# Optimization experiments

Hardware: AMD Instinct MI355X
Metric: run time of the kernel (lower is better)

The kernel has to match this reference:

```python
import jax, jax.numpy as jnp
import numpy as np

H, C, L = 4, 64, 3          # heads, out_channels, conv layers
N, E, B = 20000, 320000, 32 # nodes, edges, graphs
HD = 64                     # hidden_dim


def setup_inputs() -> dict:
    key = jax.random.key(0)
    ks = jax.random.split(key, 24)
    x = jax.random.normal(ks[0], (N, 3), jnp.float32)
    src = jax.random.randint(ks[1], (E,), 0, N)
    dst = jax.random.randint(ks[2], (E,), 0, N)
    dst = jnp.where(dst == src, (dst + 1) % N, dst)  # no pre-existing self loops
    edge_index = jnp.stack([src, dst])
    edge_attr = jax.random.normal(ks[3], (E, 4), jnp.float32)
    u = jax.random.normal(ks[4], (B, 10), jnp.float32)
    batch = jnp.sort(jax.random.randint(ks[5], (N,), 0, B))
    p = lambda k, s: jax.random.normal(k, s, jnp.float32) * 0.1
    return {
        'x': x, 'edge_index': edge_index, 'edge_attr': edge_attr, 'u': u, 'batch': batch,
        'node_W': p(ks[6], (3, HD)), 'node_b': p(ks[7], (HD,)),
        'eemb_W': p(ks[8], (4, HD)), 'eemb_b': p(ks[9], (HD,)),
        'lin_W': p(ks[10], (L, HD, H * C)),
        'att_src': p(ks[11], (L, H, C)), 'att_dst': p(ks[12], (L, H, C)),
        'lin_eW': p(ks[13], (L, HD, H * C)), 'att_e': p(ks[14], (L, H, C)),
        'conv_b': p(ks[15], (L, C)),
        'gW': p(ks[16], (10, HD)), 'gb': p(ks[17], (HD,)),
        'f1W': p(ks[18], (2 * HD, HD)), 'f1b': p(ks[19], (HD,)),
        'f2W': p(ks[20], (HD, 2)), 'f2b': p(ks[21], (2,)),
    }


def _gat_layer(x, src, dst, ea, W, a_src, a_dst, We, a_e, b):
    # PyG GATConv(hidden, hidden, edge_dim=hidden, heads=4, concat=False), eval mode
    n = x.shape[0]
    # add self loops; self-loop edge_attr = mean of incoming edge_attr (fill_value='mean')
    deg = jax.ops.segment_sum(jnp.ones_like(dst, dtype=x.dtype), dst, num_segments=n)
    ea_self = jax.ops.segment_sum(ea, dst, num_segments=n) / jnp.maximum(deg, 1.0)[:, None]
    loop = jnp.arange(n)
    src2 = jnp.concatenate([src, loop])
    dst2 = jnp.concatenate([dst, loop])
    ea2 = jnp.concatenate([ea, ea_self], axis=0)
    xp = (x @ W).reshape(n, H, C)                       # [N,H,C]
    a_s = jnp.einsum('nhc,hc->nh', xp, a_src)           # [N,H]
    a_d = jnp.einsum('nhc,hc->nh', xp, a_dst)
    ee = (ea2 @ We).reshape(-1, H, C)                   # [E2,H,C]
    a_ed = jnp.einsum('ehc,hc->eh', ee, a_e)
    alpha = jax.nn.leaky_relu(a_s[src2] + a_d[dst2] + a_ed, 0.2)  # [E2,H]
    # segment softmax over destination nodes (stable)
    m = jax.ops.segment_max(alpha, dst2, num_segments=n)
    ex = jnp.exp(alpha - m[dst2])
    den = jax.ops.segment_sum(ex, dst2, num_segments=n)
    att = ex / den[dst2]
    out = jax.ops.segment_sum(xp[src2] * att[..., None], dst2, num_segments=n)  # [N,H,C]
    return out.mean(axis=1) + b  # concat=False -> mean over heads


def reference(x, edge_index, edge_attr, u, batch, node_W, node_b, eemb_W, eemb_b,
              lin_W, att_src, att_dst, lin_eW, att_e, conv_b, gW, gb, f1W, f1b, f2W, f2b):
    src, dst = edge_index[0], edge_index[1]
    h = jax.nn.relu(x @ node_W + node_b)
    ea = jax.nn.relu(edge_attr @ eemb_W + eemb_b)
    for i in range(L):
        h = jax.nn.relu(_gat_layer(h, src, dst, ea, lin_W[i], att_src[i], att_dst[i],
                                   lin_eW[i], att_e[i], conv_b[i]))
    # global mean pool over graphs
    cnt = jax.ops.segment_sum(jnp.ones((h.shape[0],), h.dtype), batch, num_segments=B)
    pooled = jax.ops.segment_sum(h, batch, num_segments=B) / jnp.maximum(cnt, 1.0)[:, None]
    ug = jax.nn.relu(u @ gW + gb)
    z = jnp.concatenate([pooled, ug], axis=1)
    z = jax.nn.relu(z @ f1W + f1b)
    return z @ f2W + f2b
```

## Files before the change

kernel.cpp:

```cpp
#include <hip/hip_runtime.h>
#include <hip/hip_bf16.h>

#define HD 64

typedef unsigned short u16;

__device__ __forceinline__ float lrelu(float x) { return x > 0.f ? x : 0.2f * x; }
__device__ __forceinline__ int clampi(int v, int maxv) {
    return v < 0 ? 0 : (v >= maxv ? maxv - 1 : v);
}
__device__ __forceinline__ float bf2f(u16 u) {
    return __uint_as_float(((unsigned int)u) << 16);
}
__device__ __forceinline__ u16 f2bf(float f) {
    unsigned int u = __float_as_uint(f);
    unsigned int lsb = (u >> 16) & 1u;
    u += 0x7fffu + lsb;
    return (u16)(u >> 16);
}

__global__ void k_init(int* deg, int* cursor, int* gcnt, float* pooled, int N, int B) {
    int i = blockIdx.x * blockDim.x + threadIdx.x;
    if (i < N) { deg[i] = 0; cursor[i] = 0; }
    if (i < B) gcnt[i] = 0;
    if (i < B * HD) pooled[i] = 0.f;
}

__global__ void k_node_emb(const float* __restrict__ x, const float* __restrict__ W,
                           const float* __restrict__ b, float* __restrict__ h, int N) {
    int i = blockIdx.x * blockDim.x + threadIdx.x;
    if (i >= N * HD) return;
    int n = i >> 6, c = i & 63;
    float acc = b[c];
    acc = fmaf(x[n * 3 + 0], W[0 * HD + c], acc);
    acc = fmaf(x[n * 3 + 1], W[1 * HD + c], acc);
    acc = fmaf(x[n * 3 + 2], W[2 * HD + c], acc);
    h[i] = fmaxf(acc, 0.f);
}

__global__ void k_deg(const int* __restrict__ dst, int* __restrict__ deg, int E, int N) {
    int e = blockIdx.x * blockDim.x + threadIdx.x;
    if (e < E) atomicAdd(&deg[clampi(dst[e], N)], 1);
}

__global__ void k_scan1(const int* __restrict__ deg, int* __restrict__ tmp,
                        int* __restrict__ bsum, int N) {
    __shared__ int s[256];
    int tid = threadIdx.x;
    int i = blockIdx.x * 256 + tid;
    int v = (i < N) ? deg[i] : 0;
    s[tid] = v;
    __syncthreads();
    for (int off = 1; off < 256; off <<= 1) {
        int t = (tid >= off) ? s[tid - off] : 0;
        __syncthreads();
        s[tid] += t;
        __syncthreads();
    }
    if (i < N) tmp[i] = s[tid];
    if (tid == 255) bsum[blockIdx.x] = s[255];
}
__global__ void k_scan2(const int* __restrict__ bsum, int* __restrict__ boff, int nb) {
    __shared__ int s[1024];
    int tid = threadIdx.x;
    int v = (tid < nb) ? bsum[tid] : 0;
    s[tid] = v;
    __syncthreads();
    for (int off = 1; off < 1024; off <<= 1) {
        int t = (tid >= off) ? s[tid - off] : 0;
        __syncthreads();
        s[tid] += t;
        __syncthreads();
    }
    if (tid < nb) boff[tid] = s[tid] - v;
}
__global__ void k_scan3(const int* __restrict__ tmp, const int* __restrict__ boff,
                        int* __restrict__ row_ptr, int N) {
    int i = blockIdx.x * blockDim.x + threadIdx.x;
    if (i == 0) row_ptr[0] = 0;
    if (i < N) row_ptr[i + 1] = tmp[i] + boff[i >> 8];
}

__global__ void k_csr(const int* __restrict__ src, const int* __restrict__ dst,
                      const int* __restrict__ row_ptr, int* __restrict__ cursor,
                      int* __restrict__ csr_src, int* __restrict__ csr_dst,
                      int* __restrict__ csr_eid, int E, int N) {
    int e = blockIdx.x * blockDim.x + threadIdx.x;
    if (e >= E) return;
    int d = clampi(dst[e], N);
    int pos = row_ptr[d] + atomicAdd(&cursor[d], 1);
    if (pos < E) {
        csr_src[pos] = clampi(src[e], N);
        csr_dst[pos] = d;
        csr_eid[pos] = e;
    }
}

#define MAXB 2048
__global__ void k_gse(const int* __restrict__ batch, int* __restrict__ gcnt, int N, int B) {
    __shared__ int s_cnt[MAXB];
    int t = threadIdx.x;
    int Bc = B < MAXB ? B : MAXB;
    for (int i = t; i < Bc; i += blockDim.x) s_cnt[i] = 0;
    __syncthreads();
    int n = blockIdx.x * blockDim.x + t;
    if (n < N) {
        int b = clampi(batch[n], B);
        if (b < MAXB) atomicAdd(&s_cnt[b], 1);
        else atomicAdd(&gcnt[b], 1);
    }
    __syncthreads();
    for (int i = t; i < Bc; i += blockDim.x)
        if (s_cnt[i] != 0) atomicAdd(&gcnt[i], s_cnt[i]);
}

__global__ __launch_bounds__(256) void k_ee(
    const float* __restrict__ edge_attr, const float* __restrict__ eW,
    const float* __restrict__ eB, const float* __restrict__ lin_eW,
    const float* __restrict__ att_e, const int* __restrict__ csr_eid,
    float* __restrict__ aed, int E) {
    __shared__ float s_ew[256];
    __shared__ float s_eb[64];
    __shared__ float s_wred[768];
    int t = threadIdx.x;
    s_ew[t] = eW[t];
    if (t < 64) s_eb[t] = eB[t];
    for (int idx = t; idx < 768; idx += 256) {
        int l = idx >> 8, hd = idx & 255, hh = hd >> 6, d = hd & 63;
        const float* We = lin_eW + (size_t)l * HD * 256;
        const float* ae = att_e + (size_t)l * 256;
        float acc = 0.f;
        for (int c = 0; c < 64; c++)
            acc = fmaf(We[d * 256 + hh * 64 + c], ae[hh * 64 + c], acc);
        s_wred[idx] = acc;
    }
    __syncthreads();
    int j0 = (blockIdx.x * 256 + t) * 4;
    if (j0 >= E) return;
    float4 a[4];
    int nv = 0;
    #pragma unroll
    for (int q = 0; q < 4; q++) {
        int j = j0 + q;
        if (j < E) {
            a[q] = *(const float4*)(edge_attr + (size_t)csr_eid[j] * 4);
            nv = q + 1;
        } else {
            a[q] = make_float4(0.f, 0.f, 0.f, 0.f);
        }
    }
    float acc[4][12];
    #pragma unroll
    for (int q = 0; q < 4; q++)
        #pragma unroll
        for (int m = 0; m < 12; m++) acc[q][m] = 0.f;
    for (int k = 0; k < HD; k++) {
        float e0 = s_ew[k], e1 = s_ew[64 + k], e2 = s_ew[128 + k], e3 = s_ew[192 + k];
        float eb = s_eb[k];
        float w[12];
        #pragma unroll
        for (int m = 0; m < 12; m++)
            w[m] = s_wred[(m >> 2) * 256 + (m & 3) * 64 + k];
        #pragma unroll
        for (int q = 0; q < 4; q++) {
            float v = fmaf(a[q].x, e0, fmaf(a[q].y, e1,
                      fmaf(a[q].z, e2, fmaf(a[q].w, e3, eb))));
            v = fmaxf(v, 0.f);
            #pragma unroll
            for (int m = 0; m < 12; m++) acc[q][m] = fmaf(v, w[m], acc[q][m]);
        }
    }
    #pragma unroll
    for (int q = 0; q < 4; q++) {
        if (q >= nv) break;
        float* o = aed + (size_t)(j0 + q) * 12;
        #pragma unroll
        for (int m = 0; m < 12; m++) o[m] = acc[q][m];
    }
}

__global__ void k_selfed(const int* __restrict__ row_ptr, float* __restrict__ aed,
                         int E, int N) {
    int n = blockIdx.x * blockDim.x + threadIdx.x;
    if (n >= N) return;
    int r0 = row_ptr[n], r1 = row_ptr[n + 1];
    float acc[12];
    #pragma unroll
    for (int m = 0; m < 12; m++) acc[m] = 0.f;
    for (int j = r0; j < r1; j++) {
        const float* p = aed + (size_t)j * 12;
        #pragma unroll
        for (int m = 0; m < 12; m++) acc[m] += p[m];
    }
    float inv = 1.f / fmaxf((float)(r1 - r0), 1.f);
    float* o = aed + (size_t)(E + n) * 12;
    #pragma unroll
    for (int m = 0; m < 12; m++) o[m] = acc[m] * inv;
}

__global__ __launch_bounds__(256) void k_xp(
    const float* __restrict__ h, const float* __restrict__ W,
    const float* __restrict__ asrc, const float* __restrict__ adst,
    u16* __restrict__ xp, float* __restrict__ a_s, float* __restrict__ a_d, int N) {
    __shared__ float hs[8 * HD];
    int n0 = blockIdx.x * 8;
    int t = threadIdx.x;
    for (int i = t; i < 8 * HD; i += 256) {
        int nn = n0 + (i >> 6);
        hs[i] = (nn < N) ? h[(size_t)nn * HD + (i & 63)] : 0.f;
    }
    __syncthreads();
    int c = t;
    float acc[8];
    #pragma unroll
    for (int k = 0; k < 8; k++) acc[k] = 0.f;
    for (int d = 0; d < HD; d++) {
        float wv = W[d * 256 + c];
        #pragma unroll
        for (int k = 0; k < 8; k++) acc[k] = fmaf(hs[k * HD + d], wv, acc[k]);
    }
    float as_ = asrc[c], ad_ = adst[c];
    int hh = c >> 6, cc = c & 63;
    #pragma unroll
    for (int k = 0; k < 8; k++) {
        int nn = n0 + k;
        float ps = acc[k] * as_;
        float pd = acc[k] * ad_;
        #pragma unroll
        for (int o = 32; o > 0; o >>= 1) {
            ps += __shfl_xor(ps, o);
            pd += __shfl_xor(pd, o);
        }
        if (nn < N) {
            xp[(size_t)nn * 256 + c] = f2bf(acc[k]);
            if (cc == 0) { a_s[nn * 4 + hh] = ps; a_d[nn * 4 + hh] = pd; }
        }
    }
}

__global__ void k_w(const int* __restrict__ csr_src, const int* __restrict__ csr_dst,
                    const float* __restrict__ aed, const float* __restrict__ a_s,
                    const float* __restrict__ a_d, float* __restrict__ wcsr,
                    int layer, int E, int N) {
    int j = blockIdx.x * blockDim.x + threadIdx.x;
    if (j >= E + N) return;
    int s, d;
    if (j < E) { s = csr_src[j]; d = csr_dst[j]; }
    else       { s = j - E; d = s; }
    const float* p = aed + (size_t)j * 12 + layer * 4;
    float4 as4 = *(const float4*)(a_s + s * 4);
    float4 ad4 = *(const float4*)(a_d + d * 4);
    float w0 = __expf(lrelu(as4.x + ad4.x + p[0]));
    float w1 = __expf(lrelu(as4.y + ad4.y + p[1]));
    float w2 = __expf(lrelu(as4.z + ad4.z + p[2]));
    float w3 = __expf(lrelu(as4.w + ad4.w + p[3]));
    *(float4*)(wcsr + (size_t)j * 4) = make_float4(w0, w1, w2, w3);
}

__global__ __launch_bounds__(256) void k_gat(
    const u16* __restrict__ xp, const float* __restrict__ wcsr,
    const int* __restrict__ row_ptr, const int* __restrict__ csr_src,
    const float* __restrict__ convb, float* __restrict__ h_out, int N, int E) {
    int wave = threadIdx.x >> 6, lane = threadIdx.x & 63;
    int n = blockIdx.x * 4 + wave;
    if (n >= N) return;
    int g = lane >> 4, p = lane & 15;
    int r0 = row_ptr[n], r1 = row_ptr[n + 1];
    float a00 = 0.f, a01 = 0.f, a02 = 0.f, a03 = 0.f;
    float a10 = 0.f, a11 = 0.f, a12 = 0.f, a13 = 0.f;
    float a20 = 0.f, a21 = 0.f, a22 = 0.f, a23 = 0.f;
    float a30 = 0.f, a31 = 0.f, a32 = 0.f, a33 = 0.f;
    float d0 = 0.f, d1 = 0.f, d2 = 0.f, d3 = 0.f;
    if (g == 0) {
        float4 w = *(const float4*)(wcsr + (size_t)(E + n) * 4);
        const u16* row = xp + (size_t)n * 256 + p * 4;
        ushort4 v0 = *(const ushort4*)(row);
        ushort4 v1 = *(const ushort4*)(row + 64);
        ushort4 v2 = *(const ushort4*)(row + 128);
        ushort4 v3 = *(const ushort4*)(row + 192);
        d0 += w.x; d1 += w.y; d2 += w.z; d3 += w.w;
        a00 = fmaf(w.x, bf2f(v0.x), a00); a01 = fmaf(w.x, bf2f(v0.y), a01);
        a02 = fmaf(w.x, bf2f(v0.z), a02); a03 = fmaf(w.x, bf2f(v0.w), a03);
        a10 = fmaf(w.y, bf2f(v1.x), a10); a11 = fmaf(w.y, bf2f(v1.y), a11);
        a12 = fmaf(w.y, bf2f(v1.z), a12); a13 = fmaf(w.y, bf2f(v1.w), a13);
        a20 = fmaf(w.z, bf2f(v2.x), a20); a21 = fmaf(w.z, bf2f(v2.y), a21);
        a22 = fmaf(w.z, bf2f(v2.z), a22); a23 = fmaf(w.z, bf2f(v2.w), a23);
        a30 = fmaf(w.w, bf2f(v3.x), a30); a31 = fmaf(w.w, bf2f(v3.y), a31);
        a32 = fmaf(w.w, bf2f(v3.z), a32); a33 = fmaf(w.w, bf2f(v3.w), a33);
    }
    for (int j = r0 + g; j < r1; j += 4) {
        float4 w = *(const float4*)(wcsr + (size_t)j * 4);
        const u16* row = xp + (size_t)csr_src[j] * 256 + p * 4;
        ushort4 v0 = *(const ushort4*)(row);
        ushort4 v1 = *(const ushort4*)(row + 64);
        ushort4 v2 = *(const ushort4*)(row + 128);
        ushort4 v3 = *(const ushort4*)(row + 192);
        d0 += w.x; d1 += w.y; d2 += w.z; d3 += w.w;
        a00 = fmaf(w.x, bf2f(v0.x), a00); a01 = fmaf(w.x, bf2f(v0.y), a01);
        a02 = fmaf(w.x, bf2f(v0.z), a02); a03 = fmaf(w.x, bf2f(v0.w), a03);
        a10 = fmaf(w.y, bf2f(v1.x), a10); a11 = fmaf(w.y, bf2f(v1.y), a11);
        a12 = fmaf(w.y, bf2f(v1.z), a12); a13 = fmaf(w.y, bf2f(v1.w), a13);
        a20 = fmaf(w.z, bf2f(v2.x), a20); a21 = fmaf(w.z, bf2f(v2.y), a21);
        a22 = fmaf(w.z, bf2f(v2.z), a22); a23 = fmaf(w.z, bf2f(v2.w), a23);
        a30 = fmaf(w.w, bf2f(v3.x), a30); a31 = fmaf(w.w, bf2f(v3.y), a31);
        a32 = fmaf(w.w, bf2f(v3.z), a32); a33 = fmaf(w.w, bf2f(v3.w), a33);
    }
    d0 += __shfl_xor(d0, 16); d0 += __shfl_xor(d0, 32);
    d1 += __shfl_xor(d1, 16); d1 += __shfl_xor(d1, 32);
    d2 += __shfl_xor(d2, 16); d2 += __shfl_xor(d2, 32);
    d3 += __shfl_xor(d3, 16); d3 += __shfl_xor(d3, 32);
    float i0 = 1.f / d0, i1 = 1.f / d1, i2 = 1.f / d2, i3 = 1.f / d3;
    float m0 = a00 * i0 + a10 * i1 + a20 * i2 + a30 * i3;
    float m1 = a01 * i0 + a11 * i1 + a21 * i2 + a31 * i3;
    float m2 = a02 * i0 + a12 * i1 + a22 * i2 + a32 * i3;
    float m3 = a03 * i0 + a13 * i1 + a23 * i2 + a33 * i3;
    m0 += __shfl_xor(m0, 16); m0 += __shfl_xor(m0, 32);
    m1 += __shfl_xor(m1, 16); m1 += __shfl_xor(m1, 32);
    m2 += __shfl_xor(m2, 16); m2 += __shfl_xor(m2, 32);
    m3 += __shfl_xor(m3, 16); m3 += __shfl_xor(m3, 32);
    if (lane < 16) {
        int c = p * 4;
        h_out[(size_t)n * HD + c + 0] = fmaxf(0.25f * m0 + convb[c + 0], 0.f);
        h_out[(size_t)n * HD + c + 1] = fmaxf(0.25f * m1 + convb[c + 1], 0.f);
        h_out[(size_t)n * HD + c + 2] = fmaxf(0.25f * m2 + convb[c + 2], 0.f);
        h_out[(size_t)n * HD + c + 3] = fmaxf(0.25f * m3 + convb[c + 3], 0.f);
    }
}

__global__ void k_pool(const float* __restrict__ h, const int* __restrict__ batch,
                       float* __restrict__ pooled, int N, int B) {
    int i = blockIdx.x * blockDim.x + threadIdx.x;
    if (i >= N * HD) return;
    int n = i >> 6, c = i & 63;
    int b = clampi(batch[n], B);
    atomicAdd(&pooled[b * HD + c], h[i]);
}

__global__ void k_mlp(const float* __restrict__ u, const float* __restrict__ gW,
                      const float* __restrict__ gb, const float* __restrict__ pooled,
                      const int* __restrict__ gcnt, const float* __restrict__ f1W,
                      const float* __restrict__ f1b, const float* __restrict__ f2W,
                      const float* __restrict__ f2b, float* __restrict__ out, int B) {
    __shared__ float z[2 * HD];
    __shared__ float z1s[HD];
    int b = blockIdx.x, t = threadIdx.x;
    float acc = gb[t];
    for (int k = 0; k < 10; k++) acc = fmaf(u[b * 10 + k], gW[k * HD + t], acc);
    z[HD + t] = fmaxf(acc, 0.f);
    float invc = 1.f / fmaxf((float)gcnt[b], 1.f);
    z[t] = pooled[b * HD + t] * invc;
    __syncthreads();
    float a1 = f1b[t];
    for (int k = 0; k < 2 * HD; k++) a1 = fmaf(z[k], f1W[k * HD + t], a1);
    z1s[t] = fmaxf(a1, 0.f);
    __syncthreads();
    if (t < 2) {
        float o = f2b[t];
        for (int k = 0; k < HD; k++) o = fmaf(z1s[k], f2W[k * 2 + t], o);
        out[b * 2 + t] = o;
    }
}

extern "C" void kernel_launch(void* const* d_in, const int* in_sizes, int n_in,
                              void* d_out, int out_size, void* d_ws, size_t ws_size,
                              hipStream_t stream) {
    const float* x         = (const float*)d_in[0];
    const int*   ei        = (const int*)d_in[1];
    const float* edge_attr = (const float*)d_in[2];
    const float* u         = (const float*)d_in[3];
    const int*   batch     = (const int*)d_in[4];
    const float* node_W    = (const float*)d_in[5];
    const float* node_b    = (const float*)d_in[6];
    const float* eemb_W    = (const float*)d_in[7];
    const float* eemb_b    = (const float*)d_in[8];
    const float* lin_W     = (const float*)d_in[9];
    const float* att_src   = (const float*)d_in[10];
    const float* att_dst   = (const float*)d_in[11];
    const float* lin_eW    = (const float*)d_in[12];
    const float* att_e     = (const float*)d_in[13];
    const float* conv_b    = (const float*)d_in[14];
    const float* gW        = (const float*)d_in[15];
    const float* gb        = (const float*)d_in[16];
    const float* f1W       = (const float*)d_in[17];
    const float* f1b       = (const float*)d_in[18];
    const float* f2W       = (const float*)d_in[19];
    const float* f2b       = (const float*)d_in[20];

    const int N = in_sizes[0] / 3;
    const int E = in_sizes[2] / 4;
    const int B = in_sizes[3] / 10;
    const int* src = ei;
    const int* dst = ei + E;
    const int NB = (N + 255) / 256;

    float* wsf = (float*)d_ws;
    float* h       = wsf;              wsf += (size_t)N * HD;
    float* a_s     = wsf;              wsf += (size_t)N * 4;
    float* a_d     = wsf;              wsf += (size_t)N * 4;
    float* aed     = wsf;              wsf += (size_t)(E + N) * 12;
    float* wcsr    = wsf;              wsf += (size_t)(E + N) * 4;
    float* pooled  = wsf;              wsf += (size_t)B * HD;
    u16* xp = (u16*)wsf;               wsf += (size_t)N * 128;
    int* wsi = (int*)wsf;
    int* deg     = wsi;                wsi += N;
    int* row_ptr = wsi;                wsi += N + 1;
    int* cursor  = wsi;                wsi += N;
    int* tmp     = wsi;                wsi += N;
    int* bsum    = wsi;                wsi += NB + 1;
    int* boff    = wsi;                wsi += NB + 1;
    int* csr_src = wsi;                wsi += E;
    int* csr_dst = wsi;                wsi += E;
    int* csr_eid = wsi;                wsi += E;
    int* gcnt    = wsi;                wsi += B;

    k_init<<<NB, 256, 0, stream>>>(deg, cursor, gcnt, pooled, N, B);
    k_node_emb<<<(N * HD + 255) / 256, 256, 0, stream>>>(x, node_W, node_b, h, N);
    k_deg<<<(E + 255) / 256, 256, 0, stream>>>(dst, deg, E, N);
    k_scan1<<<NB, 256, 0, stream>>>(deg, tmp, bsum, N);
    k_scan2<<<1, 1024, 0, stream>>>(bsum, boff, NB);
    k_scan3<<<NB, 256, 0, stream>>>(tmp, boff, row_ptr, N);
    k_csr<<<(E + 255) / 256, 256, 0, stream>>>(src, dst, row_ptr, cursor,
                                               csr_src, csr_dst, csr_eid, E, N);
    k_gse<<<NB, 256, 0, stream>>>(batch, gcnt, N, B);
    k_ee<<<(E + 1023) / 1024, 256, 0, stream>>>(edge_attr, eemb_W, eemb_b, lin_eW, att_e,
                                                csr_eid, aed, E);
    k_selfed<<<NB, 256, 0, stream>>>(row_ptr, aed, E, N);
    for (int i = 0; i < 3; i++) {
        k_xp<<<(N + 7) / 8, 256, 0, stream>>>(h, lin_W + (size_t)i * HD * 256,
                                              att_src + (size_t)i * 256,
                                              att_dst + (size_t)i * 256,
                                              xp, a_s, a_d, N);
        k_w<<<(E + N + 255) / 256, 256, 0, stream>>>(csr_src, csr_dst, aed, a_s, a_d,
                                                     wcsr, i, E, N);
        k_gat<<<(N + 3) / 4, 256, 0, stream>>>(xp, wcsr, row_ptr, csr_src,
                                               conv_b + (size_t)i * HD, h, N, E);
    }
    k_pool<<<(N * HD + 255) / 256, 256, 0, stream>>>(h, batch, pooled, N, B);
    k_mlp<<<B, 64, 0, stream>>>(u, gW, gb, pooled, gcnt, f1W, f1b, f2W, f2b,
                                (float*)d_out, B);
}
```

Before: 413.2 us.

## Fuse attention-weight computation into GAT aggregation and pooling into last layer

Removes the separate per-edge weight kernel: the aggregation kernel now computes exp(leaky_relu(a_s+a_d+a_e)) inline for each CSR edge, dropping the wcsr buffer write and read. The last layer atomically accumulates into the pooled buffer instead of writing h and running a separate pool kernel. Init and node-embedding kernels are merged, as are degree counting and graph-size counting, cutting launch count. In exchange each of the 16 lanes in an edge group recomputes the four exps redundantly, and pooling uses more global atomics per node.

```diff
diff --git a/kernel.cpp b/kernel.cpp
--- a/kernel.cpp
+++ b/kernel.cpp
@@ -19,28 +19,43 @@
     return (u16)(u >> 16);
 }
 
-__global__ void k_init(int* deg, int* cursor, int* gcnt, float* pooled, int N, int B) {
+__global__ void k_init_emb(const float* __restrict__ x, const float* __restrict__ W,
+                           const float* __restrict__ b, float* __restrict__ h,
+                           int* deg, int* cursor, int* gcnt, float* pooled,
+                           int N, int B) {
     int i = blockIdx.x * blockDim.x + threadIdx.x;
     if (i < N) { deg[i] = 0; cursor[i] = 0; }
     if (i < B) gcnt[i] = 0;
     if (i < B * HD) pooled[i] = 0.f;
-}
-
-__global__ void k_node_emb(const float* __restrict__ x, const float* __restrict__ W,
-                           const float* __restrict__ b, float* __restrict__ h, int N) {
-    int i = blockIdx.x * blockDim.x + threadIdx.x;
-    if (i >= N * HD) return;
-    int n = i >> 6, c = i & 63;
-    float acc = b[c];
-    acc = fmaf(x[n * 3 + 0], W[0 * HD + c], acc);
-    acc = fmaf(x[n * 3 + 1], W[1 * HD + c], acc);
-    acc = fmaf(x[n * 3 + 2], W[2 * HD + c], acc);
-    h[i] = fmaxf(acc, 0.f);
-}
-
-__global__ void k_deg(const int* __restrict__ dst, int* __restrict__ deg, int E, int N) {
-    int e = blockIdx.x * blockDim.x + threadIdx.x;
-    if (e < E) atomicAdd(&deg[clampi(dst[e], N)], 1);
+    if (i < N * HD) {
+        int n = i >> 6, c = i & 63;
+        float acc = b[c];
+        acc = fmaf(x[n * 3 + 0], W[0 * HD + c], acc);
+        acc = fmaf(x[n * 3 + 1], W[1 * HD + c], acc);
+        acc = fmaf(x[n * 3 + 2], W[2 * HD + c], acc);
+        h[i] = fmaxf(acc, 0.f);
+    }
+}
+
+#define MAXB 2048
+__global__ void k_deg_gse(const int* __restrict__ dst, int* __restrict__ deg,
+                          const int* __restrict__ batch, int* __restrict__ gcnt,
+                          int E, int N, int B) {
+    __shared__ int s_cnt[MAXB];
+    int t = threadIdx.x;
+    int Bc = B < MAXB ? B : MAXB;
+    for (int i = t; i < Bc; i += blockDim.x) s_cnt[i] = 0;
+    __syncthreads();
+    int gid = blockIdx.x * blockDim.x + t;
+    if (gid < E) atomicAdd(&deg[clampi(dst[gid], N)], 1);
+    if (gid < N) {
+        int b = clampi(batch[gid], B);
+        if (b < MAXB) atomicAdd(&s_cnt[b], 1);
+        else atomicAdd(&gcnt[b], 1);
+    }
+    __syncthreads();
+    for (int i = t; i < Bc; i += blockDim.x)
+        if (s_cnt[i] != 0) atomicAdd(&gcnt[i], s_cnt[i]);
 }
 
 __global__ void k_scan1(const int* __restrict__ deg, int* __restrict__ tmp,
@@ -94,24 +109,6 @@
         csr_dst[pos] = d;
         csr_eid[pos] = e;
     }
-}
-
-#define MAXB 2048
-__global__ void k_gse(const int* __restrict__ batch, int* __restrict__ gcnt, int N, int B) {
-    __shared__ int s_cnt[MAXB];
-    int t = threadIdx.x;
-    int Bc = B < MAXB ? B : MAXB;
-    for (int i = t; i < Bc; i += blockDim.x) s_cnt[i] = 0;
-    __syncthreads();
-    int n = blockIdx.x * blockDim.x + t;
-    if (n < N) {
-        int b = clampi(batch[n], B);
-        if (b < MAXB) atomicAdd(&s_cnt[b], 1);
-        else atomicAdd(&gcnt[b], 1);
-    }
-    __syncthreads();
-    for (int i = t; i < Bc; i += blockDim.x)
-        if (s_cnt[i] != 0) atomicAdd(&gcnt[i], s_cnt[i]);
 }
 
 __global__ __launch_bounds__(256) void k_ee(
@@ -238,72 +235,68 @@
     }
 }
 
-__global__ void k_w(const int* __restrict__ csr_src, const int* __restrict__ csr_dst,
-                    const float* __restrict__ aed, const float* __restrict__ a_s,
-                    const float* __restrict__ a_d, float* __restrict__ wcsr,
-                    int layer, int E, int N) {
-    int j = blockIdx.x * blockDim.x + threadIdx.x;
-    if (j >= E + N) return;
-    int s, d;
-    if (j < E) { s = csr_src[j]; d = csr_dst[j]; }
-    else       { s = j - E; d = s; }
-    const float* p = aed + (size_t)j * 12 + layer * 4;
-    float4 as4 = *(const float4*)(a_s + s * 4);
-    float4 ad4 = *(const float4*)(a_d + d * 4);
-    float w0 = __expf(lrelu(as4.x + ad4.x + p[0]));
-    float w1 = __expf(lrelu(as4.y + ad4.y + p[1]));
-    float w2 = __expf(lrelu(as4.z + ad4.z + p[2]));
-    float w3 = __expf(lrelu(as4.w + ad4.w + p[3]));
-    *(float4*)(wcsr + (size_t)j * 4) = make_float4(w0, w1, w2, w3);
-}
-
-__global__ __launch_bounds__(256) void k_gat(
-    const u16* __restrict__ xp, const float* __restrict__ wcsr,
+__global__ __launch_bounds__(256) void k_gatw(
+    const u16* __restrict__ xp, const float* __restrict__ aed,
+    const float* __restrict__ a_s, const float* __restrict__ a_d,
     const int* __restrict__ row_ptr, const int* __restrict__ csr_src,
-    const float* __restrict__ convb, float* __restrict__ h_out, int N, int E) {
+    const float* __restrict__ convb, int layer, const int* __restrict__ batch,
+    float* __restrict__ pooled, int do_pool, float* __restrict__ h_out,
+    int N, int E, int B) {
     int wave = threadIdx.x >> 6, lane = threadIdx.x & 63;
     int n = blockIdx.x * 4 + wave;
     if (n >= N) return;
     int g = lane >> 4, p = lane & 15;
     int r0 = row_ptr[n], r1 = row_ptr[n + 1];
+    float4 ad4 = *(const float4*)(a_d + n * 4);
     float a00 = 0.f, a01 = 0.f, a02 = 0.f, a03 = 0.f;
     float a10 = 0.f, a11 = 0.f, a12 = 0.f, a13 = 0.f;
     float a20 = 0.f, a21 = 0.f, a22 = 0.f, a23 = 0.f;
     float a30 = 0.f, a31 = 0.f, a32 = 0.f, a33 = 0.f;
     float d0 = 0.f, d1 = 0.f, d2 = 0.f, d3 = 0.f;
     if (g == 0) {
-        float4 w = *(const float4*)(wcsr + (size_t)(E + n) * 4);
+        float4 as4 = *(const float4*)(a_s + n * 4);
+        float4 pe = *(const float4*)(aed + (size_t)(E + n) * 12 + layer * 4);
+        float w0 = __expf(lrelu(as4.x + ad4.x + pe.x));
+        float w1 = __expf(lrelu(as4.y + ad4.y + pe.y));
+        float w2 = __expf(lrelu(as4.z + ad4.z + pe.z));
+        float w3 = __expf(lrelu(as4.w + ad4.w + pe.w));
         const u16* row = xp + (size_t)n * 256 + p * 4;
         ushort4 v0 = *(const ushort4*)(row);
         ushort4 v1 = *(const ushort4*)(row + 64);
         ushort4 v2 = *(const ushort4*)(row + 128);
         ushort4 v3 = *(const ushort4*)(row + 192);
-        d0 += w.x; d1 += w.y; d2 += w.z; d3 += w.w;
-        a00 = fmaf(w.x, bf2f(v0.x), a00); a01 = fmaf(w.x, bf2f(v0.y), a01);
-        a02 = fmaf(w.x, bf2f(v0.z), a02); a03 = fmaf(w.x, bf2f(v0.w), a03);
-        a10 = fmaf(w.y, bf2f(v1.x), a10); a11 = fmaf(w.y, bf2f(v1.y), a11);
-        a12 = fmaf(w.y, bf2f(v1.z), a12); a13 = fmaf(w.y, bf2f(v1.w), a13);
-        a20 = fmaf(w.z, bf2f(v2.x), a20); a21 = fmaf(w.z, bf2f(v2.y), a21);
-        a22 = fmaf(w.z, bf2f(v2.z), a22); a23 = fmaf(w.z, bf2f(v2.w), a23);
-        a30 = fmaf(w.w, bf2f(v3.x), a30); a31 = fmaf(w.w, bf2f(v3.y), a31);
-        a32 = fmaf(w.w, bf2f(v3.z), a32); a33 = fmaf(w.w, bf2f(v3.w), a33);
+        d0 += w0; d1 += w1; d2 += w2; d3 += w3;
+        a00 = fmaf(w0, bf2f(v0.x), a00); a01 = fmaf(w0, bf2f(v0.y), a01);
+        a02 = fmaf(w0, bf2f(v0.z), a02); a03 = fmaf(w0, bf2f(v0.w), a03);
+        a10 = fmaf(w1, bf2f(v1.x), a10); a11 = fmaf(w1, bf2f(v1.y), a11);
+        a12 = fmaf(w1, bf2f(v1.z), a12); a13 = fmaf(w1, bf2f(v1.w), a13);
+        a20 = fmaf(w2, bf2f(v2.x), a20); a21 = fmaf(w2, bf2f(v2.y), a21);
+        a22 = fmaf(w2, bf2f(v2.z), a22); a23 = fmaf(w2, bf2f(v2.w), a23);
+        a30 = fmaf(w3, bf2f(v3.x), a30); a31 = fmaf(w3, bf2f(v3.y), a31);
+        a32 = fmaf(w3, bf2f(v3.z), a32); a33 = fmaf(w3, bf2f(v3.w), a33);
     }
     for (int j = r0 + g; j < r1; j += 4) {
-        float4 w = *(const float4*)(wcsr + (size_t)j * 4);
-        const u16* row = xp + (size_t)csr_src[j] * 256 + p * 4;
+        int s = csr_src[j];
+        float4 as4 = *(const float4*)(a_s + s * 4);
+        float4 pe = *(const float4*)(aed + (size_t)j * 12 + layer * 4);
+        float w0 = __expf(lrelu(as4.x + ad4.x + pe.x));
+        float w1 = __expf(lrelu(as4.y + ad4.y + pe.y));
+        float w2 = __expf(lrelu(as4.z + ad4.z + pe.z));
+        float w3 = __expf(lrelu(as4.w + ad4.w + pe.w));
+        const u16* row = xp + (size_t)s * 256 + p * 4;
         ushort4 v0 = *(const ushort4*)(row);
         ushort4 v1 = *(const ushort4*)(row + 64);
         ushort4 v2 = *(const ushort4*)(row + 128);
         ushort4 v3 = *(const ushort4*)(row + 192);
-        d0 += w.x; d1 += w.y; d2 += w.z; d3 += w.w;
-        a00 = fmaf(w.x, bf2f(v0.x), a00); a01 = fmaf(w.x, bf2f(v0.y), a01);
-        a02 = fmaf(w.x, bf2f(v0.z), a02); a03 = fmaf(w.x, bf2f(v0.w), a03);
-        a10 = fmaf(w.y, bf2f(v1.x), a10); a11 = fmaf(w.y, bf2f(v1.y), a11);
-        a12 = fmaf(w.y, bf2f(v1.z), a12); a13 = fmaf(w.y, bf2f(v1.w), a13);
-        a20 = fmaf(w.z, bf2f(v2.x), a20); a21 = fmaf(w.z, bf2f(v2.y), a21);
-        a22 = fmaf(w.z, bf2f(v2.z), a22); a23 = fmaf(w.z, bf2f(v2.w), a23);
-        a30 = fmaf(w.w, bf2f(v3.x), a30); a31 = fmaf(w.w, bf2f(v3.y), a31);
-        a32 = fmaf(w.w, bf2f(v3.z), a32); a33 = fmaf(w.w, bf2f(v3.w), a33);
+        d0 += w0; d1 += w1; d2 += w2; d3 += w3;
+        a00 = fmaf(w0, bf2f(v0.x), a00); a01 = fmaf(w0, bf2f(v0.y), a01);
+        a02 = fmaf(w0, bf2f(v0.z), a02); a03 = fmaf(w0, bf2f(v0.w), a03);
+        a10 = fmaf(w1, bf2f(v1.x), a10); a11 = fmaf(w1, bf2f(v1.y), a11);
+        a12 = fmaf(w1, bf2f(v1.z), a12); a13 = fmaf(w1, bf2f(v1.w), a13);
+        a20 = fmaf(w2, bf2f(v2.x), a20); a21 = fmaf(w2, bf2f(v2.y), a21);
+        a22 = fmaf(w2, bf2f(v2.z), a22); a23 = fmaf(w2, bf2f(v2.w), a23);
+        a30 = fmaf(w3, bf2f(v3.x), a30); a31 = fmaf(w3, bf2f(v3.y), a31);
+        a32 = fmaf(w3, bf2f(v3.z), a32); a33 = fmaf(w3, bf2f(v3.w), a33);
     }
     d0 += __shfl_xor(d0, 16); d0 += __shfl_xor(d0, 32);
     d1 += __shfl_xor(d1, 16); d1 += __shfl_xor(d1, 32);
@@ -320,20 +313,23 @@
     m3 += __shfl_xor(m3, 16); m3 += __shfl_xor(m3, 32);
     if (lane < 16) {
         int c = p * 4;
-        h_out[(size_t)n * HD + c + 0] = fmaxf(0.25f * m0 + convb[c + 0], 0.f);
-        h_out[(size_t)n * HD + c + 1] = fmaxf(0.25f * m1 + convb[c + 1], 0.f);
-        h_out[(size_t)n * HD + c + 2] = fmaxf(0.25f * m2 + convb[c + 2], 0.f);
-        h_out[(size_t)n * HD + c + 3] = fmaxf(0.25f * m3 + convb[c + 3], 0.f);
-    }
-}
-
-__global__ void k_pool(const float* __restrict__ h, const int* __restrict__ batch,
-                       float* __restrict__ pooled, int N, int B) {
-    int i = blockIdx.x * blockDim.x + threadIdx.x;
-    if (i >= N * HD) return;
-    int n = i >> 6, c = i & 63;
-    int b = clampi(batch[n], B);
-    atomicAdd(&pooled[b * HD + c], h[i]);
+        float o0 = fmaxf(0.25f * m0 + convb[c + 0], 0.f);
+        float o1 = fmaxf(0.25f * m1 + convb[c + 1], 0.f);
+        float o2 = fmaxf(0.25f * m2 + convb[c + 2], 0.f);
+        float o3 = fmaxf(0.25f * m3 + convb[c + 3], 0.f);
+        if (do_pool) {
+            int b = clampi(batch[n], B);
+            atomicAdd(&pooled[b * HD + c + 0], o0);
+            atomicAdd(&pooled[b * HD + c + 1], o1);
+            atomicAdd(&pooled[b * HD + c + 2], o2);
+            atomicAdd(&pooled[b * HD + c + 3], o3);
+        } else {
+            h_out[(size_t)n * HD + c + 0] = o0;
+            h_out[(size_t)n * HD + c + 1] = o1;
+            h_out[(size_t)n * HD + c + 2] = o2;
+            h_out[(size_t)n * HD + c + 3] = o3;
+        }
+    }
 }
 
 __global__ void k_mlp(const float* __restrict__ u, const float* __restrict__ gW,
@@ -392,13 +388,13 @@
     const int* src = ei;
     const int* dst = ei + E;
     const int NB = (N + 255) / 256;
+    const int MEN = (E > N ? E : N);
 
     float* wsf = (float*)d_ws;
     float* h       = wsf;              wsf += (size_t)N * HD;
     float* a_s     = wsf;              wsf += (size_t)N * 4;
     float* a_d     = wsf;              wsf += (size_t)N * 4;
     float* aed     = wsf;              wsf += (size_t)(E + N) * 12;
-    float* wcsr    = wsf;              wsf += (size_t)(E + N) * 4;
     float* pooled  = wsf;              wsf += (size_t)B * HD;
     u16* xp = (u16*)wsf;               wsf += (size_t)N * 128;
     int* wsi = (int*)wsf;
@@ -413,15 +409,14 @@
     int* csr_eid = wsi;                wsi += E;
     int* gcnt    = wsi;                wsi += B;
 
-    k_init<<<NB, 256, 0, stream>>>(deg, cursor, gcnt, pooled, N, B);
-    k_node_emb<<<(N * HD + 255) / 256, 256, 0, stream>>>(x, node_W, node_b, h, N);
-    k_deg<<<(E + 255) / 256, 256, 0, stream>>>(dst, deg, E, N);
+    k_init_emb<<<(N * HD + 255) / 256, 256, 0, stream>>>(x, node_W, node_b, h,
+                                                         deg, cursor, gcnt, pooled, N, B);
+    k_deg_gse<<<(MEN + 255) / 256, 256, 0, stream>>>(dst, deg, batch, gcnt, E, N, B);
     k_scan1<<<NB, 256, 0, stream>>>(deg, tmp, bsum, N);
     k_scan2<<<1, 1024, 0, stream>>>(bsum, boff, NB);
     k_scan3<<<NB, 256, 0, stream>>>(tmp, boff, row_ptr, N);
     k_csr<<<(E + 255) / 256, 256, 0, stream>>>(src, dst, row_ptr, cursor,
                                                csr_src, csr_dst, csr_eid, E, N);
-    k_gse<<<NB, 256, 0, stream>>>(batch, gcnt, N, B);
     k_ee<<<(E + 1023) / 1024, 256, 0, stream>>>(edge_attr, eemb_W, eemb_b, lin_eW, att_e,
                                                 csr_eid, aed, E);
     k_selfed<<<NB, 256, 0, stream>>>(row_ptr, aed, E, N);
@@ -430,12 +425,10 @@
                                               att_src + (size_t)i * 256,
                                               att_dst + (size_t)i * 256,
                                               xp, a_s, a_d, N);
-        k_w<<<(E + N + 255) / 256, 256, 0, stream>>>(csr_src, csr_dst, aed, a_s, a_d,
-                                                     wcsr, i, E, N);
-        k_gat<<<(N + 3) / 4, 256, 0, stream>>>(xp, wcsr, row_ptr, csr_src,
-                                               conv_b + (size_t)i * HD, h, N, E);
-    }
-    k_pool<<<(N * HD + 255) / 256, 256, 0, stream>>>(h, batch, pooled, N, B);
+        k_gatw<<<(N + 3) / 4, 256, 0, stream>>>(xp, aed, a_s, a_d, row_ptr, csr_src,
+                                                conv_b + (size_t)i * HD, i, batch, pooled,
+                                                (i == 2) ? 1 : 0, h, N, E, B);
+    }
     k_mlp<<<B, 64, 0, stream>>>(u, gW, gb, pooled, gcnt, f1W, f1b, f2W, f2b,
                                 (float*)d_out, B);
 }
```

New measurement: 501.0 us. +21.3%, slower.
